# Performance work log

Hardware: AMD Instinct MI355X
Metric: run time of the kernel (lower is better)

The kernel has to match this reference:

```python
import jax, jax.numpy as jnp
import numpy as np

N, INP, H, FH = 768, 256, 4, 64  # nodes, inp_dim, heads, hidden-per-head (out_dim=H*FH=256)


def setup_inputs() -> dict:
    key = jax.random.key(0)
    k1, k2, k3, k4 = jax.random.split(key, 4)
    x = jax.random.normal(k1, (N, INP), dtype=jnp.float32)
    adj_mat = jax.random.randint(k2, (N, N, 1), 0, 2, dtype=jnp.int32)
    # nn.Linear weights: W.weight [H*FH, INP], a.weight [1, FH] (stored as [FH])
    W = jax.random.uniform(k3, (H * FH, INP), dtype=jnp.float32, minval=-0.1, maxval=0.1)
    a = jax.random.uniform(k4, (FH,), dtype=jnp.float32, minval=-0.1, maxval=0.1)
    return {"x": x, "adj_mat": adj_mat, "W": W, "a": a}


def reference(x, adj_mat, W, a):
    n = x.shape[0]
    Wx = (x @ W.T).reshape(n, H, FH)                       # [N,H,F]
    # dense pairwise features: Wx_ij[i,j] = Wx[i] + Wx[j] (symmetric sum)
    s = Wx[:, None, :, :] + Wx[None, :, :, :]             # [N,N,H,F]
    # dynamic attention: a(leaky_relu(Wx_ij))
    e = jnp.einsum('ijhf,f->ijh', jax.nn.leaky_relu(s, 0.2), a)  # [N,N,H]
    e = jnp.where(adj_mat == 0, -jnp.inf, e)               # adj [N,N,1] broadcasts over H
    att = jax.nn.softmax(e, axis=1)                        # softmax over neighbors j
    # dropout is identity in eval/reference mode
    xh = jnp.einsum('ijh,jhf->ihf', att, Wx)               # [N,H,F]
    return xh.reshape(n, H * FH)                           # concat heads
```

## Files before the change

### kernel.cpp

```cpp
#include <hip/hip_runtime.h>
#include <hip/hip_bf16.h>

#define NN   768
#define INP  256
#define NH   4
#define FH   64
#define DOUT 256

__device__ __forceinline__ float b2f(unsigned short u) {
    union { unsigned int i; float f; } v;
    v.i = ((unsigned int)u) << 16;
    return v.f;
}
__device__ __forceinline__ unsigned short f2b(float f) {
    union { float f; unsigned int i; } v; v.f = f;
    unsigned int lsb = (v.i >> 16) & 1;
    v.i += 0x7FFFu + lsb;
    return (unsigned short)(v.i >> 16);
}

__device__ __forceinline__ int detect_bf16(const void* xin) {
    const unsigned int* xw = (const unsigned int*)xin;
    unsigned int u = xw[(threadIdx.x & 63) * 7];
    unsigned int e = (u >> 7) & 0xFFu;
    unsigned long long m = __ballot(e >= 124u && e <= 127u);
    return (__popcll(m) >= 32) ? 1 : 0;
}

__global__ __launch_bounds__(256) void wx_kernel(
    const void* __restrict__ xin, const void* __restrict__ Win,
    const void* __restrict__ ain,
    unsigned short* __restrict__ Wxh, float* __restrict__ lin,
    float* __restrict__ af32, int* __restrict__ flagout)
{
    const int isbf = detect_bf16(xin);
    __shared__ float xs[4][INP];
    const int tid = threadIdx.x;
    const int r0  = blockIdx.x * 4;

    if (isbf) {
        const unsigned short* xp = (const unsigned short*)xin + r0 * INP;
        for (int idx = tid; idx < 4 * INP; idx += 256)
            xs[idx >> 8][idx & 255] = b2f(xp[idx]);
    } else {
        const float* xp = (const float*)xin + r0 * INP;
        for (int idx = tid; idx < 4 * INP; idx += 256)
            xs[idx >> 8][idx & 255] = xp[idx];
    }
    __syncthreads();

    const int o = tid;
    float acc0 = 0.f, acc1 = 0.f, acc2 = 0.f, acc3 = 0.f;
    if (isbf) {
        const unsigned short* wr = (const unsigned short*)Win + o * INP;
        #pragma unroll 4
        for (int k = 0; k < INP; k += 4) {
            ushort4 u = *(const ushort4*)(wr + k);
            float4 w = make_float4(b2f(u.x), b2f(u.y), b2f(u.z), b2f(u.w));
            float4 x0 = *(const float4*)&xs[0][k];
            float4 x1 = *(const float4*)&xs[1][k];
            float4 x2 = *(const float4*)&xs[2][k];
            float4 x3 = *(const float4*)&xs[3][k];
            acc0 += x0.x * w.x + x0.y * w.y + x0.z * w.z + x0.w * w.w;
            acc1 += x1.x * w.x + x1.y * w.y + x1.z * w.z + x1.w * w.w;
            acc2 += x2.x * w.x + x2.y * w.y + x2.z * w.z + x2.w * w.w;
            acc3 += x3.x * w.x + x3.y * w.y + x3.z * w.z + x3.w * w.w;
        }
    } else {
        const float* wr = (const float*)Win + o * INP;
        #pragma unroll 4
        for (int k = 0; k < INP; k += 4) {
            float4 w = *(const float4*)(wr + k);
            float4 x0 = *(const float4*)&xs[0][k];
            float4 x1 = *(const float4*)&xs[1][k];
            float4 x2 = *(const float4*)&xs[2][k];
            float4 x3 = *(const float4*)&xs[3][k];
            acc0 += x0.x * w.x + x0.y * w.y + x0.z * w.z + x0.w * w.w;
            acc1 += x1.x * w.x + x1.y * w.y + x1.z * w.z + x1.w * w.w;
            acc2 += x2.x * w.x + x2.y * w.y + x2.z * w.z + x2.w * w.w;
            acc3 += x3.x * w.x + x3.y * w.y + x3.z * w.z + x3.w * w.w;
        }
    }

    Wxh[(r0 + 0) * DOUT + o] = f2b(acc0);
    Wxh[(r0 + 1) * DOUT + o] = f2b(acc1);
    Wxh[(r0 + 2) * DOUT + o] = f2b(acc2);
    Wxh[(r0 + 3) * DOUT + o] = f2b(acc3);

    const int f = tid & 63;
    const int h = tid >> 6;
    const float av = isbf ? b2f(((const unsigned short*)ain)[f])
                          : ((const float*)ain)[f];
    if (blockIdx.x == 0) {
        if (tid < 64) af32[tid] = av;
        if (tid == 0) *flagout = isbf;
    }

    const float af = 0.6f * av;
    float v0 = af * acc0, v1 = af * acc1, v2 = af * acc2, v3 = af * acc3;
    #pragma unroll
    for (int d = 1; d < 64; d <<= 1) {
        v0 += __shfl_xor(v0, d);
        v1 += __shfl_xor(v1, d);
        v2 += __shfl_xor(v2, d);
        v3 += __shfl_xor(v3, d);
    }
    if (f == 0) {
        lin[(r0 + 0) * NH + h] = v0;
        lin[(r0 + 1) * NH + h] = v1;
        lin[(r0 + 2) * NH + h] = v2;
        lin[(r0 + 3) * NH + h] = v3;
    }
}

__global__ __launch_bounds__(256) void attn_kernel(
    const unsigned short* __restrict__ Wxh,
    const float* __restrict__ lin,
    const int* __restrict__ adj,
    const float* __restrict__ af32,
    void* __restrict__ outv,
    const int* __restrict__ flag)
{
    __shared__ float att[NH][NN];
    __shared__ unsigned short jlist[NN];
    __shared__ int cnt;

    const int i    = blockIdx.x;
    const int tid  = threadIdx.x;
    const int wv   = tid >> 6;
    const int lane = tid & 63;
    const int jq   = lane >> 4;
    const int fg   = lane & 15;
    const int isbf = *flag;

    if (tid == 0) cnt = 0;

    float4 wi[NH];
    #pragma unroll
    for (int h = 0; h < NH; ++h) {
        ushort4 u = *(const ushort4*)(Wxh + i * DOUT + h * FH + fg * 4);
        wi[h] = make_float4(b2f(u.x), b2f(u.y), b2f(u.z), b2f(u.w));
    }
    float4 a4;
    {
        const float4 av = *(const float4*)(af32 + fg * 4);
        a4 = make_float4(0.4f * av.x, 0.4f * av.y, 0.4f * av.z, 0.4f * av.w);
    }
    float lini[NH];
    #pragma unroll
    for (int h = 0; h < NH; ++h) lini[h] = lin[i * NH + h];

    __syncthreads();

    const int* adjrow = adj + i * NN;
    #pragma unroll
    for (int t = 0; t < 3; ++t) {
        const int j = wv * 192 + t * 64 + lane;
        const bool act = adjrow[j] != 0;
        const unsigned long long m = __ballot(act);
        const int pre = __popcll(m & ((1ull << lane) - 1ull));
        int base = 0;
        if (lane == 0) base = atomicAdd(&cnt, __popcll(m));
        base = __shfl(base, 0);
        if (act) jlist[base + pre] = (unsigned short)j;
    }
    __syncthreads();
    const int count = cnt;

    for (int base = 0; base < count; base += 16) {
        const int s = base + wv * 4 + jq;
        if (s < count) {
            const int j = jlist[s];
            const unsigned short* wjp = Wxh + j * DOUT + fg * 4;
            float ev[NH];
            #pragma unroll
            for (int h = 0; h < NH; ++h) {
                ushort4 u = *(const ushort4*)(wjp + h * FH);
                float x0 = wi[h].x + b2f(u.x);
                float x1 = wi[h].y + b2f(u.y);
                float x2 = wi[h].z + b2f(u.z);
                float x3 = wi[h].w + b2f(u.w);
                float sv = a4.x * fabsf(x0) + a4.y * fabsf(x1)
                         + a4.z * fabsf(x2) + a4.w * fabsf(x3);
                sv += __shfl_xor(sv, 1);
                sv += __shfl_xor(sv, 2);
                sv += __shfl_xor(sv, 4);
                sv += __shfl_xor(sv, 8);
                ev[h] = sv;
            }
            if (fg == 0) {
                const float4 lj = *(const float4*)(lin + j * NH);
                att[0][s] = lini[0] + lj.x + ev[0];
                att[1][s] = lini[1] + lj.y + ev[1];
                att[2][s] = lini[2] + lj.z + ev[2];
                att[3][s] = lini[3] + lj.w + ev[3];
            }
        }
    }
    __syncthreads();

    const int h = wv;
    float m = -__builtin_inff();
    for (int s = lane; s < count; s += 64) m = fmaxf(m, att[h][s]);
    #pragma unroll
    for (int d = 1; d < 64; d <<= 1) m = fmaxf(m, __shfl_xor(m, d));
    float ssum = 0.f;
    for (int s = lane; s < count; s += 64) {
        const float v = __expf(att[h][s] - m);
        att[h][s] = v;
        ssum += v;
    }
    #pragma unroll
    for (int d = 1; d < 64; d <<= 1) ssum += __shfl_xor(ssum, d);
    const float inv = (count > 0) ? 1.f / ssum : 0.f;
    __syncthreads();

    const unsigned short* colbase = Wxh + h * FH + lane;
    float acc = 0.f;
    int s4 = 0;
    for (; s4 + 4 <= count; s4 += 4) {
        const float4  w  = *(const float4*)&att[h][s4];
        const ushort4 jj = *(const ushort4*)&jlist[s4];
        acc += w.x * b2f(colbase[(int)jj.x * DOUT]);
        acc += w.y * b2f(colbase[(int)jj.y * DOUT]);
        acc += w.z * b2f(colbase[(int)jj.z * DOUT]);
        acc += w.w * b2f(colbase[(int)jj.w * DOUT]);
    }
    for (; s4 < count; ++s4)
        acc += att[h][s4] * b2f(colbase[(int)jlist[s4] * DOUT]);
    acc *= inv;

    if (isbf) ((unsigned short*)outv)[i * DOUT + tid] = f2b(acc);
    else      ((float*)outv)[i * DOUT + tid] = acc;
}

extern "C" void kernel_launch(void* const* d_in, const int* in_sizes, int n_in,
                              void* d_out, int out_size, void* d_ws, size_t ws_size,
                              hipStream_t stream) {
    const void* px = d_in[0]; const void* padj = d_in[1];
    const void* pW = d_in[2]; const void* pa  = d_in[3];
    for (int t = 0; t < n_in; ++t) {
        switch (in_sizes[t]) {
            case NN * INP:   px   = d_in[t]; break;
            case NN * NN:    padj = d_in[t]; break;
            case DOUT * INP: pW   = d_in[t]; break;
            case FH:         pa   = d_in[t]; break;
        }
    }

    char* ws = (char*)d_ws;
    int*            flag = (int*)ws;
    float*          af32 = (float*)(ws + 256);
    unsigned short* Wxh  = (unsigned short*)(ws + 512);
    float*          lin  = (float*)(ws + 512 + 393216);

    wx_kernel<<<NN / 4, 256, 0, stream>>>(px, pW, pa, Wxh, lin, af32, flag);
    attn_kernel<<<NN, 256, 0, stream>>>(Wxh, lin, (const int*)padj, af32, d_out, flag);
}
```

Measured before the change: 108.1 us.

## Split attention into dense fp16 score kernel and MFMA softmax-aggregate kernel

Replaces the per-node sparse gather attention kernel with two kernels. The first computes dense masked scores for all head/node pairs using packed fp16 adds and fdot2 on j-tiles held in shared memory. The second does the softmax and multiplies the result by a transposed fp16 Wx copy using 16x16x32 f16 MFMA instructions. The data also moves from bf16 to fp16, which adds an N*N*H fp16 scratch buffer and an extra launch, and may change numerical precision.

```diff
diff --git a/kernel.cpp b/kernel.cpp
--- a/kernel.cpp
+++ b/kernel.cpp
@@ -7,6 +7,13 @@
 #define FH   64
 #define DOUT 256
 
+typedef _Float16 h2 __attribute__((ext_vector_type(2)));
+typedef _Float16 h8 __attribute__((ext_vector_type(8)));
+typedef float    f4 __attribute__((ext_vector_type(4)));
+
+union HU { unsigned int u; h2 h; };
+union HS { _Float16 h; unsigned short s; };
+
 __device__ __forceinline__ float b2f(unsigned short u) {
     union { unsigned int i; float f; } v;
     v.i = ((unsigned int)u) << 16;
@@ -17,6 +24,23 @@
     unsigned int lsb = (v.i >> 16) & 1;
     v.i += 0x7FFFu + lsb;
     return (unsigned short)(v.i >> 16);
+}
+
+__device__ __forceinline__ unsigned int pkadd(unsigned int a, unsigned int b) {
+    HU x, y, r; x.u = a; y.u = b; r.h = x.h + y.h; return r.u;
+}
+#if defined(__has_builtin)
+#if __has_builtin(__builtin_amdgcn_fdot2)
+#define HAVE_FDOT2 1
+#endif
+#endif
+__device__ __forceinline__ float dot2abs(unsigned int a, unsigned int s, float acc) {
+    HU x, y; x.u = a; y.u = s & 0x7FFF7FFFu;
+#ifdef HAVE_FDOT2
+    return __builtin_amdgcn_fdot2(x.h, y.h, acc, false);
+#else
+    return acc + (float)x.h.x * (float)y.h.x + (float)x.h.y * (float)y.h.y;
+#endif
 }
 
 __device__ __forceinline__ int detect_bf16(const void* xin) {
@@ -30,11 +54,13 @@
 __global__ __launch_bounds__(256) void wx_kernel(
     const void* __restrict__ xin, const void* __restrict__ Win,
     const void* __restrict__ ain,
-    unsigned short* __restrict__ Wxh, float* __restrict__ lin,
-    float* __restrict__ af32, int* __restrict__ flagout)
+    _Float16* __restrict__ Wxf, _Float16* __restrict__ BT,
+    float* __restrict__ lin, unsigned int* __restrict__ apk,
+    int* __restrict__ flagout)
 {
     const int isbf = detect_bf16(xin);
     __shared__ float xs[4][INP];
+    __shared__ float sa[64];
     const int tid = threadIdx.x;
     const int r0  = blockIdx.x * 4;
 
@@ -47,6 +73,9 @@
         for (int idx = tid; idx < 4 * INP; idx += 256)
             xs[idx >> 8][idx & 255] = xp[idx];
     }
+    if (tid < 64)
+        sa[tid] = isbf ? b2f(((const unsigned short*)ain)[tid])
+                       : ((const float*)ain)[tid];
     __syncthreads();
 
     const int o = tid;
@@ -82,21 +111,30 @@
         }
     }
 
-    Wxh[(r0 + 0) * DOUT + o] = f2b(acc0);
-    Wxh[(r0 + 1) * DOUT + o] = f2b(acc1);
-    Wxh[(r0 + 2) * DOUT + o] = f2b(acc2);
-    Wxh[(r0 + 3) * DOUT + o] = f2b(acc3);
+    Wxf[(r0 + 0) * DOUT + o] = (_Float16)acc0;
+    Wxf[(r0 + 1) * DOUT + o] = (_Float16)acc1;
+    Wxf[(r0 + 2) * DOUT + o] = (_Float16)acc2;
+    Wxf[(r0 + 3) * DOUT + o] = (_Float16)acc3;
+    {
+        HU u0, u1;
+        u0.h = h2{(_Float16)acc0, (_Float16)acc1};
+        u1.h = h2{(_Float16)acc2, (_Float16)acc3};
+        uint2 pv; pv.x = u0.u; pv.y = u1.u;
+        *(uint2*)(BT + (size_t)o * NN + r0) = pv;
+    }
 
     const int f = tid & 63;
     const int h = tid >> 6;
-    const float av = isbf ? b2f(((const unsigned short*)ain)[f])
-                          : ((const float*)ain)[f];
     if (blockIdx.x == 0) {
-        if (tid < 64) af32[tid] = av;
         if (tid == 0) *flagout = isbf;
-    }
-
-    const float af = 0.6f * av;
+        if (tid < 32) {
+            HU p; p.h = h2{(_Float16)(0.4f * sa[2 * tid]),
+                           (_Float16)(0.4f * sa[2 * tid + 1])};
+            apk[tid] = p.u;
+        }
+    }
+
+    const float af = 0.6f * sa[f];
     float v0 = af * acc0, v1 = af * acc1, v2 = af * acc2, v3 = af * acc3;
     #pragma unroll
     for (int d = 1; d < 64; d <<= 1) {
@@ -113,125 +151,128 @@
     }
 }
 
-__global__ __launch_bounds__(256) void attn_kernel(
-    const unsigned short* __restrict__ Wxh,
+#define ROWP 264
+__global__ __launch_bounds__(256, 2) void e_kernel(
+    const _Float16* __restrict__ Wxf,
     const float* __restrict__ lin,
+    const unsigned int* __restrict__ apk,
     const int* __restrict__ adj,
-    const float* __restrict__ af32,
+    _Float16* __restrict__ eH)
+{
+    __shared__ __align__(16) unsigned short wt[64 * ROWP];
+
+    const int b    = blockIdx.x;
+    const int jt   = b % 12, it = b / 12;
+    const int i0   = it * 8, j0 = jt * 64;
+    const int tid  = threadIdx.x;
+    const int h    = tid >> 6;
+    const int lane = tid & 63;
+
+    for (int t = tid; t < 64 * 32; t += 256) {
+        const int row = t >> 5, c = t & 31;
+        const uint4 v = *(const uint4*)(Wxf + (size_t)(j0 + row) * DOUT + c * 8);
+        *(uint4*)(&wt[row * ROWP + c * 8]) = v;
+    }
+    __syncthreads();
+
+    uint4 wj[8], ap[8];
+    #pragma unroll
+    for (int c = 0; c < 8; ++c)
+        wj[c] = *(const uint4*)(&wt[lane * ROWP + h * FH + c * 8]);
+    #pragma unroll
+    for (int c = 0; c < 8; ++c)
+        ap[c] = *(const uint4*)(apk + c * 4);
+
+    const float linj = lin[(j0 + lane) * NH + h];
+    const unsigned short NEGINF = 0xFC00;
+
+    #pragma unroll
+    for (int ii = 0; ii < 8; ++ii) {
+        const int i = i0 + ii;
+        const float lini = lin[i * NH + h];
+        const int adjv = adj[(size_t)i * NN + j0 + lane];
+        float acc = 0.f;
+        #pragma unroll
+        for (int c = 0; c < 8; ++c) {
+            const uint4 wiv = *(const uint4*)(Wxf + (size_t)i * DOUT + h * FH + c * 8);
+            acc = dot2abs(ap[c].x, pkadd(wiv.x, wj[c].x), acc);
+            acc = dot2abs(ap[c].y, pkadd(wiv.y, wj[c].y), acc);
+            acc = dot2abs(ap[c].z, pkadd(wiv.z, wj[c].z), acc);
+            acc = dot2abs(ap[c].w, pkadd(wiv.w, wj[c].w), acc);
+        }
+        const float ev = acc + lini + linj;
+        HS hv; hv.h = (_Float16)ev;
+        unsigned short st = adjv ? hv.s : NEGINF;
+        ((unsigned short*)eH)[((size_t)h * NN + i) * NN + j0 + lane] = st;
+    }
+}
+
+#define KP 776
+__global__ __launch_bounds__(256) void av_kernel(
+    const _Float16* __restrict__ eH,
+    const _Float16* __restrict__ BT,
     void* __restrict__ outv,
     const int* __restrict__ flag)
 {
-    __shared__ float att[NH][NN];
-    __shared__ unsigned short jlist[NN];
-    __shared__ int cnt;
-
-    const int i    = blockIdx.x;
+    __shared__ __align__(16) _Float16 P[16][KP];
+    __shared__ float S[16];
+
+    const int b    = blockIdx.x;
+    const int h    = b & 3, it = b >> 2;
+    const int i0   = it * 16;
     const int tid  = threadIdx.x;
     const int wv   = tid >> 6;
     const int lane = tid & 63;
-    const int jq   = lane >> 4;
-    const int fg   = lane & 15;
+
+    #pragma unroll
+    for (int rr = 0; rr < 4; ++rr) {
+        const int row = wv * 4 + rr;
+        const _Float16* er = eH + ((size_t)h * NN + i0 + row) * NN;
+        float v[12];
+        float m = -__builtin_inff();
+        #pragma unroll
+        for (int c = 0; c < 12; ++c) {
+            v[c] = (float)er[c * 64 + lane];
+            m = fmaxf(m, v[c]);
+        }
+        #pragma unroll
+        for (int d = 1; d < 64; d <<= 1) m = fmaxf(m, __shfl_xor(m, d));
+        if (m == -__builtin_inff()) m = 0.f;
+        float s = 0.f;
+        #pragma unroll
+        for (int c = 0; c < 12; ++c) {
+            const float ev = __expf(v[c] - m);
+            s += ev;
+            P[row][c * 64 + lane] = (_Float16)ev;
+        }
+        #pragma unroll
+        for (int d = 1; d < 64; d <<= 1) s += __shfl_xor(s, d);
+        if (lane == 0) S[row] = fmaxf(s, 1e-30f);
+    }
+    __syncthreads();
+
+    const int mrow = lane & 15;
+    const int quad = lane >> 4;
+    const int n0   = wv * 16;
+    f4 acc = {0.f, 0.f, 0.f, 0.f};
+    const _Float16* bbase = BT + ((size_t)(h * FH + n0 + mrow)) * NN + quad * 8;
+    const _Float16* abase = &P[mrow][quad * 8];
+    #pragma unroll 4
+    for (int k0 = 0; k0 < NN; k0 += 32) {
+        const h8 af = *(const h8*)(abase + k0);
+        const h8 bf = *(const h8*)(bbase + k0);
+        acc = __builtin_amdgcn_mfma_f32_16x16x32_f16(af, bf, acc, 0, 0, 0);
+    }
+
     const int isbf = *flag;
-
-    if (tid == 0) cnt = 0;
-
-    float4 wi[NH];
-    #pragma unroll
-    for (int h = 0; h < NH; ++h) {
-        ushort4 u = *(const ushort4*)(Wxh + i * DOUT + h * FH + fg * 4);
-        wi[h] = make_float4(b2f(u.x), b2f(u.y), b2f(u.z), b2f(u.w));
-    }
-    float4 a4;
-    {
-        const float4 av = *(const float4*)(af32 + fg * 4);
-        a4 = make_float4(0.4f * av.x, 0.4f * av.y, 0.4f * av.z, 0.4f * av.w);
-    }
-    float lini[NH];
-    #pragma unroll
-    for (int h = 0; h < NH; ++h) lini[h] = lin[i * NH + h];
-
-    __syncthreads();
-
-    const int* adjrow = adj + i * NN;
-    #pragma unroll
-    for (int t = 0; t < 3; ++t) {
-        const int j = wv * 192 + t * 64 + lane;
-        const bool act = adjrow[j] != 0;
-        const unsigned long long m = __ballot(act);
-        const int pre = __popcll(m & ((1ull << lane) - 1ull));
-        int base = 0;
-        if (lane == 0) base = atomicAdd(&cnt, __popcll(m));
-        base = __shfl(base, 0);
-        if (act) jlist[base + pre] = (unsigned short)j;
-    }
-    __syncthreads();
-    const int count = cnt;
-
-    for (int base = 0; base < count; base += 16) {
-        const int s = base + wv * 4 + jq;
-        if (s < count) {
-            const int j = jlist[s];
-            const unsigned short* wjp = Wxh + j * DOUT + fg * 4;
-            float ev[NH];
-            #pragma unroll
-            for (int h = 0; h < NH; ++h) {
-                ushort4 u = *(const ushort4*)(wjp + h * FH);
-                float x0 = wi[h].x + b2f(u.x);
-                float x1 = wi[h].y + b2f(u.y);
-                float x2 = wi[h].z + b2f(u.z);
-                float x3 = wi[h].w + b2f(u.w);
-                float sv = a4.x * fabsf(x0) + a4.y * fabsf(x1)
-                         + a4.z * fabsf(x2) + a4.w * fabsf(x3);
-                sv += __shfl_xor(sv, 1);
-                sv += __shfl_xor(sv, 2);
-                sv += __shfl_xor(sv, 4);
-                sv += __shfl_xor(sv, 8);
-                ev[h] = sv;
-            }
-            if (fg == 0) {
-                const float4 lj = *(const float4*)(lin + j * NH);
-                att[0][s] = lini[0] + lj.x + ev[0];
-                att[1][s] = lini[1] + lj.y + ev[1];
-                att[2][s] = lini[2] + lj.z + ev[2];
-                att[3][s] = lini[3] + lj.w + ev[3];
-            }
-        }
-    }
-    __syncthreads();
-
-    const int h = wv;
-    float m = -__builtin_inff();
-    for (int s = lane; s < count; s += 64) m = fmaxf(m, att[h][s]);
-    #pragma unroll
-    for (int d = 1; d < 64; d <<= 1) m = fmaxf(m, __shfl_xor(m, d));
-    float ssum = 0.f;
-    for (int s = lane; s < count; s += 64) {
-        const float v = __expf(att[h][s] - m);
-        att[h][s] = v;
-        ssum += v;
-    }
-    #pragma unroll
-    for (int d = 1; d < 64; d <<= 1) ssum += __shfl_xor(ssum, d);
-    const float inv = (count > 0) ? 1.f / ssum : 0.f;
-    __syncthreads();
-
-    const unsigned short* colbase = Wxh + h * FH + lane;
-    float acc = 0.f;
-    int s4 = 0;
-    for (; s4 + 4 <= count; s4 += 4) {
-        const float4  w  = *(const float4*)&att[h][s4];
-        const ushort4 jj = *(const ushort4*)&jlist[s4];
-        acc += w.x * b2f(colbase[(int)jj.x * DOUT]);
-        acc += w.y * b2f(colbase[(int)jj.y * DOUT]);
-        acc += w.z * b2f(colbase[(int)jj.z * DOUT]);
-        acc += w.w * b2f(colbase[(int)jj.w * DOUT]);
-    }
-    for (; s4 < count; ++s4)
-        acc += att[h][s4] * b2f(colbase[(int)jlist[s4] * DOUT]);
-    acc *= inv;
-
-    if (isbf) ((unsigned short*)outv)[i * DOUT + tid] = f2b(acc);
-    else      ((float*)outv)[i * DOUT + tid] = acc;
+    #pragma unroll
+    for (int r = 0; r < 4; ++r) {
+        const int row = quad * 4 + r;
+        const float val = acc[r] / S[row];
+        const size_t oidx = (size_t)(i0 + row) * DOUT + h * FH + n0 + mrow;
+        if (isbf) ((unsigned short*)outv)[oidx] = f2b(val);
+        else      ((float*)outv)[oidx] = val;
+    }
 }
 
 extern "C" void kernel_launch(void* const* d_in, const int* in_sizes, int n_in,
@@ -249,11 +290,15 @@
     }
 
     char* ws = (char*)d_ws;
-    int*            flag = (int*)ws;
-    float*          af32 = (float*)(ws + 256);
-    unsigned short* Wxh  = (unsigned short*)(ws + 512);
-    float*          lin  = (float*)(ws + 512 + 393216);
-
-    wx_kernel<<<NN / 4, 256, 0, stream>>>(px, pW, pa, Wxh, lin, af32, flag);
-    attn_kernel<<<NN, 256, 0, stream>>>(Wxh, lin, (const int*)padj, af32, d_out, flag);
-}
+    int*          flag = (int*)ws;
+    unsigned int* apk  = (unsigned int*)(ws + 256);
+    float*        lin  = (float*)(ws + 1024);
+    _Float16*     Wxf  = (_Float16*)(ws + 16384);
+    _Float16*     BT   = (_Float16*)(ws + 409600);
+    _Float16*     eH   = (_Float16*)(ws + 802816);
+
+    wx_kernel<<<NN / 4, 256, 0, stream>>>(px, pW, pa, Wxf, BT, lin, apk, flag);
+    e_kernel<<<(NN / 8) * (NN / 64), 256, 0, stream>>>(Wxf, lin, apk,
+                                                       (const int*)padj, eH);
+    av_kernel<<<(NN / 16) * NH, 256, 0, stream>>>(eH, BT, d_out, flag);
+}
```

Result: faster. 98.84 us (-8.6%).
